# Kernel tuning notes

Measured on AMD Instinct MI355X. Metric: run time of the kernel, lower is better.

The kernel has to match this reference:

```python
import jax, jax.numpy as jnp
import numpy as np

N_NODES = 100000
N_EDGES = 1600000
IN_F = 256
OUT_F = 128


def setup_inputs() -> dict:
    key = jax.random.key(0)
    k1, k2, k3, k4, k5, k6 = jax.random.split(key, 6)
    x = jax.random.normal(k1, (N_NODES, IN_F), dtype=jnp.float32)
    edge_row = jax.random.randint(k2, (N_EDGES,), 0, N_NODES, dtype=jnp.int32)
    edge_col = jax.random.randint(k3, (N_EDGES,), 0, N_NODES, dtype=jnp.int32)
    edge_val = jax.random.uniform(k4, (N_EDGES,), dtype=jnp.float32)
    # xavier_uniform for W: bound = sqrt(6/(fan_in+fan_out))
    bound_w = float(np.sqrt(6.0 / (IN_F + OUT_F)))
    W = jax.random.uniform(k5, (IN_F, OUT_F), dtype=jnp.float32, minval=-bound_w, maxval=bound_w)
    stdv = 1.0 / float(np.sqrt(OUT_F))
    b = jax.random.uniform(k6, (OUT_F,), dtype=jnp.float32, minval=-stdv, maxval=stdv)
    return {"x": x, "edge_row": edge_row, "edge_col": edge_col, "edge_val": edge_val, "W": W, "b": b}


def reference(x, edge_row, edge_col, edge_val, W, b):
    # dropout p=0.0 -> identity
    support = x @ W + b                      # [N, out]
    # sparse adjacency matmul: out[r] += val * support[c] over edges (r, c, val)
    msgs = edge_val[:, None] * support[edge_col]          # [E, out]
    out = jax.ops.segment_sum(msgs, edge_row, num_segments=N_NODES)  # [N, out]
    return jax.nn.relu(out)
```

## Files before the change

### kernel.cpp

```cpp
#include <hip/hip_runtime.h>


constexpr int kNodes = 100000;
constexpr int kEdges = 1600000;
constexpr int kInF   = 256;
constexpr int kOutF  = 128;
constexpr int kTiles = kNodes / 16;
constexpr int kGemmBlocks = 1250;

constexpr int kNB  = 1024;
constexpr int kRB  = 98;
constexpr int kCap = 1792;
constexpr int kBinBlocks = 256;
constexpr int kEPB = kEdges / kBinBlocks;

constexpr int kTileCap = 1024;

typedef __attribute__((ext_vector_type(8))) short short8;
typedef __attribute__((ext_vector_type(8))) unsigned short ush8;
typedef __attribute__((ext_vector_type(4))) float floatx4;

__device__ inline unsigned short f2bf_rne(float f) {
    unsigned int u = __float_as_uint(f);
    unsigned int r = u + 0x7FFFu + ((u >> 16) & 1u);
    return (unsigned short)(r >> 16);
}
__device__ inline float bf2f(unsigned short h) {
    return __uint_as_float(((unsigned int)h) << 16);
}

__device__ inline short8 cvt8_bf16(const float4 a, const float4 b) {
    union { short8 s; unsigned int u[4]; } r;
    asm("v_cvt_pk_bf16_f32 %0, %1, %2" : "=v"(r.u[0]) : "v"(a.x), "v"(a.y));
    asm("v_cvt_pk_bf16_f32 %0, %1, %2" : "=v"(r.u[1]) : "v"(a.z), "v"(a.w));
    asm("v_cvt_pk_bf16_f32 %0, %1, %2" : "=v"(r.u[2]) : "v"(b.x), "v"(b.y));
    asm("v_cvt_pk_bf16_f32 %0, %1, %2" : "=v"(r.u[3]) : "v"(b.z), "v"(b.w));
    return r.s;
}

__device__ inline void gload_lds16(const void* g, void* l) {
    __builtin_amdgcn_global_load_lds(
        (const __attribute__((address_space(1))) unsigned int*)g,
        (__attribute__((address_space(3))) unsigned int*)l,
        16, 0, 0);
}

__global__ __launch_bounds__(256) void gcn_gemm(const float* __restrict__ x,
                                                const float* __restrict__ W,
                                                const float* __restrict__ b,
                                                unsigned short* __restrict__ support) {
    __shared__ __align__(16) float lbuf[2][4096];

    const int lane = threadIdx.x & 63;
    const int wv   = threadIdx.x >> 6;
    const int rowl = lane & 15;
    const int quad = lane >> 4;
    const int colbase = wv * 32;

    short8 bfrag[2][8];
#pragma unroll
    for (int ct = 0; ct < 2; ++ct) {
        const int col = colbase + ct * 16 + rowl;
#pragma unroll
        for (int kc = 0; kc < 8; ++kc) {
            const int kb = kc * 32 + quad * 8;
            short8 f;
#pragma unroll
            for (int j = 0; j < 8; ++j)
                f[j] = (short)f2bf_rne(W[(size_t)(kb + j) * kOutF + col]);
            bfrag[ct][kc] = f;
        }
    }
    const float bias0 = b[colbase + rowl];
    const float bias1 = b[colbase + 16 + rowl];

    const int G = gridDim.x;
    int t = blockIdx.x;

#define GEMM_STAGE(buf_, tile_)                                                   \
    do {                                                                          \
        const float* tb_ = x + (size_t)(tile_) * 16 * kInF;                       \
        _Pragma("unroll")                                                         \
        for (int i_ = 0; i_ < 4; ++i_) {                                          \
            const int row_ = i_ * 4 + wv;                                         \
            gload_lds16(tb_ + (size_t)row_ * kInF + ((lane ^ (row_ & 7)) << 2),   \
                        &lbuf[buf_][row_ << 8]);                                  \
        }                                                                         \
    } while (0)

    if (t < kTiles) GEMM_STAGE(0, t);
    int cur = 0;

    for (; t < kTiles; t += G) {
        const int tn = t + G;
        asm volatile("s_waitcnt vmcnt(0)" ::: "memory");
        __syncthreads();
        if (tn < kTiles) GEMM_STAGE(cur ^ 1, tn);

        const int r0 = t * 16;
        const float* base = &lbuf[cur][rowl << 8];
        const int rsw = rowl & 7;
        floatx4 acc0 = {0.f, 0.f, 0.f, 0.f};
        floatx4 acc1 = {0.f, 0.f, 0.f, 0.f};
#pragma unroll
        for (int kc = 0; kc < 8; ++kc) {
            const int g0 = (kc << 3) + (quad << 1);
            const float4 v0 = *reinterpret_cast<const float4*>(base + ((g0 ^ rsw) << 2));
            const float4 v1 = *reinterpret_cast<const float4*>(base + (((g0 + 1) ^ rsw) << 2));
            const short8 a = cvt8_bf16(v0, v1);
            acc0 = __builtin_amdgcn_mfma_f32_16x16x32_bf16(a, bfrag[0][kc], acc0, 0, 0, 0);
            acc1 = __builtin_amdgcn_mfma_f32_16x16x32_bf16(a, bfrag[1][kc], acc1, 0, 0, 0);
        }
#pragma unroll
        for (int reg = 0; reg < 4; ++reg) {
            const size_t rbase = (size_t)(r0 + quad * 4 + reg) * kOutF + colbase;
            support[rbase + rowl]      = f2bf_rne(acc0[reg] + bias0);
            support[rbase + 16 + rowl] = f2bf_rne(acc1[reg] + bias1);
        }
        cur ^= 1;
    }
#undef GEMM_STAGE
}

__global__ __launch_bounds__(256) void gcn_bhist(const int* __restrict__ erow,
                                                 int* __restrict__ bucket_tot) {
    __shared__ int cnt[kNB];
    const int tid = threadIdx.x;
    for (int i = tid; i < kNB; i += 256) cnt[i] = 0;
    __syncthreads();
    const int eb0 = blockIdx.x * kEPB;
    const int eb1 = min(eb0 + kEPB, kEdges);
    for (int e = eb0 + tid; e < eb1; e += 256)
        atomicAdd(&cnt[(unsigned int)erow[e] / (unsigned int)kRB], 1);
    __syncthreads();
    for (int i = tid; i < kNB; i += 256) {
        const int c = cnt[i];
        if (c) atomicAdd(&bucket_tot[i], c);
    }
}

__global__ __launch_bounds__(256) void gcn_bscan(const int* __restrict__ bucket_tot,
                                                 int* __restrict__ bucket_base,
                                                 int* __restrict__ cursor,
                                                 int* __restrict__ row_start) {
    __shared__ int s[kNB];
    const int tid = threadIdx.x;
    int t[4];
#pragma unroll
    for (int j = 0; j < 4; ++j) {
        const int idx = tid + j * 256;
        t[j] = bucket_tot[idx];
        s[idx] = t[j];
    }
    __syncthreads();
    for (int off = 1; off < kNB; off <<= 1) {
        int v[4];
#pragma unroll
        for (int j = 0; j < 4; ++j) {
            const int idx = tid + j * 256;
            v[j] = (idx >= off) ? s[idx - off] : 0;
        }
        __syncthreads();
#pragma unroll
        for (int j = 0; j < 4; ++j) s[tid + j * 256] += v[j];
        __syncthreads();
    }
#pragma unroll
    for (int j = 0; j < 4; ++j) {
        const int idx = tid + j * 256;
        const int excl = s[idx] - t[j];
        bucket_base[idx] = excl;
        cursor[idx]      = excl;
    }
    if (tid == 255) {
        bucket_base[kNB]  = kEdges;
        row_start[kNodes] = kEdges;
    }
}

__global__ __launch_bounds__(256) void gcn_bin(const int* __restrict__ erow,
                                               const int* __restrict__ ecol,
                                               const float* __restrict__ eval,
                                               int* __restrict__ cursor,
                                               int2* __restrict__ packed) {
    __shared__ int cnt[kNB];
    __shared__ int rk[kNB];
    const int tid = threadIdx.x;
    const int eb0 = blockIdx.x * kEPB;
    const int eb1 = min(eb0 + kEPB, kEdges);
    for (int i = tid; i < kNB; i += 256) { cnt[i] = 0; rk[i] = 0; }
    __syncthreads();
#pragma unroll 4
    for (int e = eb0 + tid; e < eb1; e += 256)
        atomicAdd(&cnt[(unsigned int)erow[e] / (unsigned int)kRB], 1);
    __syncthreads();
    for (int i = tid; i < kNB; i += 256) {
        const int c = cnt[i];
        cnt[i] = c ? atomicAdd(&cursor[i], c) : 0;
    }
    __syncthreads();
#pragma unroll 4
    for (int e = eb0 + tid; e < eb1; e += 256) {
        const int r = erow[e];
        const unsigned int bk = (unsigned int)r / (unsigned int)kRB;
        const int rl = r - (int)bk * kRB;
        const int pos = cnt[bk] + atomicAdd(&rk[bk], 1);
        packed[pos] = make_int2((rl << 17) | ecol[e], __float_as_int(eval[e]));
    }
}

__global__ __launch_bounds__(256) void gcn_place(const int* __restrict__ bucket_base,
                                                 int* __restrict__ row_start,
                                                 int2* __restrict__ packed) {
    __shared__ int2 st[kCap];
    __shared__ int  s[128];
    __shared__ int  rcur[kRB];
    const int bk = blockIdx.x;
    const int r0 = bk * kRB;
    if (r0 >= kNodes) return;
    const int r1 = min(r0 + kRB, kNodes);
    const int NR = r1 - r0;
    const int bb = bucket_base[bk];
    const int s1 = bucket_base[bk + 1];
    const int size   = s1 - bb;
    const int staged = min(size, kCap);
    const int tid = threadIdx.x;

    if (tid < 128) s[tid] = 0;
    __syncthreads();

    for (int i = tid; i < staged; i += 256) {
        const int2 p = packed[bb + i];
        st[i] = p;
        atomicAdd(&s[p.x >> 17], 1);
    }
    int2 tail[8];
    int  nt = 0;
    for (int i = kCap + tid; i < size; i += 256) {
        if (nt < 8) {
            tail[nt] = packed[bb + i];
            atomicAdd(&s[tail[nt].x >> 17], 1);
            ++nt;
        }
    }
    __syncthreads();

    for (int off = 1; off < 128; off <<= 1) {
        int v = 0;
        if (tid < 128 && tid >= off) v = s[tid - off];
        __syncthreads();
        if (tid < 128) s[tid] += v;
        __syncthreads();
    }
    if (tid < NR) {
        const int excl = tid ? s[tid - 1] : 0;
        row_start[r0 + tid] = bb + excl;
        rcur[tid] = excl;
    }
    __syncthreads();

    for (int i = tid; i < staged; i += 256) {
        const int2 p  = st[i];
        const int pos = bb + atomicAdd(&rcur[p.x >> 17], 1);
        packed[pos] = make_int2(p.x & 0x1FFFF, p.y);
    }
#pragma unroll
    for (int t = 0; t < 8; ++t) {
        if (t < nt) {
            const int2 p  = tail[t];
            const int pos = bb + atomicAdd(&rcur[p.x >> 17], 1);
            packed[pos] = make_int2(p.x & 0x1FFFF, p.y);
        }
    }
}

__global__ __launch_bounds__(256) void gcn_aggregate(const int* __restrict__ row_start,
                                                     const int2* __restrict__ packed,
                                                     const unsigned short* __restrict__ support,
                                                     float* __restrict__ out) {
    __shared__ int2 ep[kTileCap];
    const int n0 = blockIdx.x * 16;
    const int e0 = row_start[n0];
    const int eN = row_start[n0 + 16] - e0;
    const int nStage = min(eN, kTileCap);
    for (int i = threadIdx.x; i < nStage; i += 256)
        ep[i] = packed[e0 + i];
    __syncthreads();

    const int n  = n0 + (threadIdx.x >> 4);
    const int f8 = (threadIdx.x & 15) * 8;
    const unsigned short* sb = support + f8;
    const int s0 = row_start[n]     - e0;
    const int s1 = row_start[n + 1] - e0;

    float acc[8];
#pragma unroll
    for (int j = 0; j < 8; ++j) acc[j] = 0.f;

    if (eN <= kTileCap) {
        int i = s0;
        for (; i + 7 < s1; i += 8) {
            int2 p[8];
#pragma unroll
            for (int k = 0; k < 8; ++k) p[k] = ep[i + k];
            ush8 g[8];
#pragma unroll
            for (int k = 0; k < 8; ++k)
                g[k] = *reinterpret_cast<const ush8*>(sb + (size_t)p[k].x * kOutF);
#pragma unroll
            for (int k = 0; k < 8; ++k) {
                const float v = __int_as_float(p[k].y);
#pragma unroll
                for (int j = 0; j < 8; ++j) acc[j] += v * bf2f(g[k][j]);
            }
        }
        for (; i < s1; ++i) {
            const int2 p = ep[i];
            const float v = __int_as_float(p.y);
            const ush8 g = *reinterpret_cast<const ush8*>(sb + (size_t)p.x * kOutF);
#pragma unroll
            for (int j = 0; j < 8; ++j) acc[j] += v * bf2f(g[j]);
        }
    } else {
        int i = s0;
        for (; i + 3 < s1; i += 4) {
            const int2 p0 = packed[e0 + i];
            const int2 p1 = packed[e0 + i + 1];
            const int2 p2 = packed[e0 + i + 2];
            const int2 p3 = packed[e0 + i + 3];
            const ush8 a0 = *reinterpret_cast<const ush8*>(sb + (size_t)p0.x * kOutF);
            const ush8 a1 = *reinterpret_cast<const ush8*>(sb + (size_t)p1.x * kOutF);
            const ush8 a2 = *reinterpret_cast<const ush8*>(sb + (size_t)p2.x * kOutF);
            const ush8 a3 = *reinterpret_cast<const ush8*>(sb + (size_t)p3.x * kOutF);
            const float v0 = __int_as_float(p0.y), v1 = __int_as_float(p1.y);
            const float v2 = __int_as_float(p2.y), v3 = __int_as_float(p3.y);
#pragma unroll
            for (int j = 0; j < 8; ++j) {
                acc[j] += v0 * bf2f(a0[j]);
                acc[j] += v1 * bf2f(a1[j]);
                acc[j] += v2 * bf2f(a2[j]);
                acc[j] += v3 * bf2f(a3[j]);
            }
        }
        for (; i < s1; ++i) {
            const int2 p = packed[e0 + i];
            const float v = __int_as_float(p.y);
            const ush8 a = *reinterpret_cast<const ush8*>(sb + (size_t)p.x * kOutF);
#pragma unroll
            for (int j = 0; j < 8; ++j) acc[j] += v * bf2f(a[j]);
        }
    }

    float4 o0 = make_float4(fmaxf(acc[0], 0.f), fmaxf(acc[1], 0.f),
                            fmaxf(acc[2], 0.f), fmaxf(acc[3], 0.f));
    float4 o1 = make_float4(fmaxf(acc[4], 0.f), fmaxf(acc[5], 0.f),
                            fmaxf(acc[6], 0.f), fmaxf(acc[7], 0.f));
    *reinterpret_cast<float4*>(out + (size_t)n * kOutF + f8)     = o0;
    *reinterpret_cast<float4*>(out + (size_t)n * kOutF + f8 + 4) = o1;
}

extern "C" void kernel_launch(void* const* d_in, const int* in_sizes, int n_in,
                              void* d_out, int out_size, void* d_ws, size_t ws_size,
                              hipStream_t stream) {
    const float* x    = (const float*)d_in[0];
    const int*   erow = (const int*)  d_in[1];
    const int*   ecol = (const int*)  d_in[2];
    const float* eval = (const float*)d_in[3];
    const float* W    = (const float*)d_in[4];
    const float* b    = (const float*)d_in[5];
    float* out = (float*)d_out;

    char* ws = (char*)d_ws;
    unsigned short* support = (unsigned short*)(ws);
    int2* packed      = (int2*)(ws + 25600000);
    int*  row_start   = (int*) (ws + 38400000);
    int*  bucket_tot  = (int*) (ws + 38800008);
    int*  bucket_base = (int*) (ws + 38804104);
    int*  cursor      = (int*) (ws + 38808204);

    gcn_gemm<<<kGemmBlocks, 256, 0, stream>>>(x, W, b, support);

    hipMemsetAsync(bucket_tot, 0, kNB * sizeof(int), stream);
    gcn_bhist<<<kBinBlocks, 256, 0, stream>>>(erow, bucket_tot);
    gcn_bscan<<<1, 256, 0, stream>>>(bucket_tot, bucket_base, cursor, row_start);
    gcn_bin  <<<kBinBlocks, 256, 0, stream>>>(erow, ecol, eval, cursor, packed);
    gcn_place<<<kNB, 256, 0, stream>>>(bucket_base, row_start, packed);

    gcn_aggregate<<<kTiles, 256, 0, stream>>>(row_start, packed, support, out);
}
```

Baseline: 331.5 us.

## Split GEMM tiles across the binning kernels to overlap compute with sorting

Removes the standalone GEMM launch and spreads its row tiles over the four CSR-build kernels (histogram, scan, bin, place). Each of these kernels gets extra blocks that run a slice of the GEMM, so the dense compute fills the idle CUs left by the small, latency-bound sorting stages. Every fused kernel now uses 32KB of dynamic shared memory, which may lower occupancy for the binning blocks. The per-stage tile splits are hand-tuned constants.

```diff
diff --git a/kernel.cpp b/kernel.cpp
--- a/kernel.cpp
+++ b/kernel.cpp
@@ -6,7 +6,6 @@
 constexpr int kInF   = 256;
 constexpr int kOutF  = 128;
 constexpr int kTiles = kNodes / 16;
-constexpr int kGemmBlocks = 1250;
 
 constexpr int kNB  = 1024;
 constexpr int kRB  = 98;
@@ -15,6 +14,10 @@
 constexpr int kEPB = kEdges / kBinBlocks;
 
 constexpr int kTileCap = 1024;
+
+constexpr int kC1 = 1600, kC2 = 1900, kC3 = 4700, kC4 = kTiles;
+constexpr int kG1 = 320, kG2 = 64, kG3 = 560, kG4 = 312;
+constexpr int kSmem = 32768;
 
 typedef __attribute__((ext_vector_type(8))) short short8;
 typedef __attribute__((ext_vector_type(8))) unsigned short ush8;
@@ -45,12 +48,11 @@
         16, 0, 0);
 }
 
-__global__ __launch_bounds__(256) void gcn_gemm(const float* __restrict__ x,
-                                                const float* __restrict__ W,
-                                                const float* __restrict__ b,
-                                                unsigned short* __restrict__ support) {
-    __shared__ __align__(16) float lbuf[2][4096];
-
+__device__ inline void gemm_body(const float* __restrict__ x,
+                                 const float* __restrict__ W,
+                                 const float* __restrict__ b,
+                                 unsigned short* __restrict__ support,
+                                 float* lbuf, int t0, int t1, int gblk, int nG) {
     const int lane = threadIdx.x & 63;
     const int wv   = threadIdx.x >> 6;
     const int rowl = lane & 15;
@@ -74,31 +76,31 @@
     const float bias0 = b[colbase + rowl];
     const float bias1 = b[colbase + 16 + rowl];
 
-    const int G = gridDim.x;
-    int t = blockIdx.x;
-
-#define GEMM_STAGE(buf_, tile_)                                                   \
+    float* bcur = lbuf;
+    float* bnxt = lbuf + 4096;
+
+#define GEMM_STAGE(dst_, tile_)                                                   \
     do {                                                                          \
         const float* tb_ = x + (size_t)(tile_) * 16 * kInF;                       \
         _Pragma("unroll")                                                         \
         for (int i_ = 0; i_ < 4; ++i_) {                                          \
             const int row_ = i_ * 4 + wv;                                         \
             gload_lds16(tb_ + (size_t)row_ * kInF + ((lane ^ (row_ & 7)) << 2),   \
-                        &lbuf[buf_][row_ << 8]);                                  \
+                        (dst_) + (row_ << 8));                                    \
         }                                                                         \
     } while (0)
 
-    if (t < kTiles) GEMM_STAGE(0, t);
-    int cur = 0;
-
-    for (; t < kTiles; t += G) {
-        const int tn = t + G;
+    int t = t0 + gblk;
+    if (t < t1) GEMM_STAGE(bcur, t);
+
+    for (; t < t1; t += nG) {
+        const int tn = t + nG;
         asm volatile("s_waitcnt vmcnt(0)" ::: "memory");
         __syncthreads();
-        if (tn < kTiles) GEMM_STAGE(cur ^ 1, tn);
+        if (tn < t1) GEMM_STAGE(bnxt, tn);
 
         const int r0 = t * 16;
-        const float* base = &lbuf[cur][rowl << 8];
+        const float* base = bcur + (rowl << 8);
         const int rsw = rowl & 7;
         floatx4 acc0 = {0.f, 0.f, 0.f, 0.f};
         floatx4 acc1 = {0.f, 0.f, 0.f, 0.f};
@@ -117,14 +119,13 @@
             support[rbase + rowl]      = f2bf_rne(acc0[reg] + bias0);
             support[rbase + 16 + rowl] = f2bf_rne(acc1[reg] + bias1);
         }
-        cur ^= 1;
+        float* tmp = bcur; bcur = bnxt; bnxt = tmp;
     }
 #undef GEMM_STAGE
 }
 
-__global__ __launch_bounds__(256) void gcn_bhist(const int* __restrict__ erow,
-                                                 int* __restrict__ bucket_tot) {
-    __shared__ int cnt[kNB];
+__device__ inline void bhist_body(const int* __restrict__ erow,
+                                  int* __restrict__ bucket_tot, int* cnt) {
     const int tid = threadIdx.x;
     for (int i = tid; i < kNB; i += 256) cnt[i] = 0;
     __syncthreads();
@@ -139,11 +140,10 @@
     }
 }
 
-__global__ __launch_bounds__(256) void gcn_bscan(const int* __restrict__ bucket_tot,
-                                                 int* __restrict__ bucket_base,
-                                                 int* __restrict__ cursor,
-                                                 int* __restrict__ row_start) {
-    __shared__ int s[kNB];
+__device__ inline void bscan_body(const int* __restrict__ bucket_tot,
+                                  int* __restrict__ bucket_base,
+                                  int* __restrict__ cursor,
+                                  int* __restrict__ row_start, int* s) {
     const int tid = threadIdx.x;
     int t[4];
 #pragma unroll
@@ -178,13 +178,11 @@
     }
 }
 
-__global__ __launch_bounds__(256) void gcn_bin(const int* __restrict__ erow,
-                                               const int* __restrict__ ecol,
-                                               const float* __restrict__ eval,
-                                               int* __restrict__ cursor,
-                                               int2* __restrict__ packed) {
-    __shared__ int cnt[kNB];
-    __shared__ int rk[kNB];
+__device__ inline void bin_body(const int* __restrict__ erow,
+                                const int* __restrict__ ecol,
+                                const float* __restrict__ eval,
+                                int* __restrict__ cursor,
+                                int2* __restrict__ packed, int* cnt, int* rk) {
     const int tid = threadIdx.x;
     const int eb0 = blockIdx.x * kEPB;
     const int eb1 = min(eb0 + kEPB, kEdges);
@@ -209,12 +207,12 @@
     }
 }
 
-__global__ __launch_bounds__(256) void gcn_place(const int* __restrict__ bucket_base,
-                                                 int* __restrict__ row_start,
-                                                 int2* __restrict__ packed) {
-    __shared__ int2 st[kCap];
-    __shared__ int  s[128];
-    __shared__ int  rcur[kRB];
+__device__ inline void place_body(const int* __restrict__ bucket_base,
+                                  int* __restrict__ row_start,
+                                  int2* __restrict__ packed, char* smem) {
+    int2* st   = (int2*)smem;
+    int*  s    = (int*)(smem + 14336);
+    int*  rcur = (int*)(smem + 14848);
     const int bk = blockIdx.x;
     const int r0 = bk * kRB;
     if (r0 >= kNodes) return;
@@ -272,6 +270,64 @@
             packed[pos] = make_int2(p.x & 0x1FFFF, p.y);
         }
     }
+}
+
+__global__ __launch_bounds__(256) void gcn_k1(const float* __restrict__ x,
+                                              const float* __restrict__ W,
+                                              const float* __restrict__ b,
+                                              unsigned short* __restrict__ support,
+                                              const int* __restrict__ erow,
+                                              int* __restrict__ bucket_tot) {
+    extern __shared__ char smem[];
+    if (blockIdx.x < kBinBlocks)
+        bhist_body(erow, bucket_tot, (int*)smem);
+    else
+        gemm_body(x, W, b, support, (float*)smem, 0, kC1, blockIdx.x - kBinBlocks, kG1);
+}
+
+__global__ __launch_bounds__(256) void gcn_k2(const float* __restrict__ x,
+                                              const float* __restrict__ W,
+                                              const float* __restrict__ b,
+                                              unsigned short* __restrict__ support,
+                                              const int* __restrict__ bucket_tot,
+                                              int* __restrict__ bucket_base,
+                                              int* __restrict__ cursor,
+                                              int* __restrict__ row_start) {
+    extern __shared__ char smem[];
+    if (blockIdx.x == 0)
+        bscan_body(bucket_tot, bucket_base, cursor, row_start, (int*)smem);
+    else
+        gemm_body(x, W, b, support, (float*)smem, kC1, kC2, blockIdx.x - 1, kG2);
+}
+
+__global__ __launch_bounds__(256) void gcn_k3(const float* __restrict__ x,
+                                              const float* __restrict__ W,
+                                              const float* __restrict__ b,
+                                              unsigned short* __restrict__ support,
+                                              const int* __restrict__ erow,
+                                              const int* __restrict__ ecol,
+                                              const float* __restrict__ eval,
+                                              int* __restrict__ cursor,
+                                              int2* __restrict__ packed) {
+    extern __shared__ char smem[];
+    if (blockIdx.x < kBinBlocks)
+        bin_body(erow, ecol, eval, cursor, packed, (int*)smem, (int*)(smem + 4096));
+    else
+        gemm_body(x, W, b, support, (float*)smem, kC2, kC3, blockIdx.x - kBinBlocks, kG3);
+}
+
+__global__ __launch_bounds__(256) void gcn_k4(const float* __restrict__ x,
+                                              const float* __restrict__ W,
+                                              const float* __restrict__ b,
+                                              unsigned short* __restrict__ support,
+                                              const int* __restrict__ bucket_base,
+                                              int* __restrict__ row_start,
+                                              int2* __restrict__ packed) {
+    extern __shared__ char smem[];
+    if (blockIdx.x < kNB)
+        place_body(bucket_base, row_start, packed, smem);
+    else
+        gemm_body(x, W, b, support, (float*)smem, kC3, kC4, blockIdx.x - kNB, kG4);
 }
 
 __global__ __launch_bounds__(256) void gcn_aggregate(const int* __restrict__ row_start,
@@ -378,13 +434,15 @@
     int*  bucket_base = (int*) (ws + 38804104);
     int*  cursor      = (int*) (ws + 38808204);
 
-    gcn_gemm<<<kGemmBlocks, 256, 0, stream>>>(x, W, b, support);
-
     hipMemsetAsync(bucket_tot, 0, kNB * sizeof(int), stream);
-    gcn_bhist<<<kBinBlocks, 256, 0, stream>>>(erow, bucket_tot);
-    gcn_bscan<<<1, 256, 0, stream>>>(bucket_tot, bucket_base, cursor, row_start);
-    gcn_bin  <<<kBinBlocks, 256, 0, stream>>>(erow, ecol, eval, cursor, packed);
-    gcn_place<<<kNB, 256, 0, stream>>>(bucket_base, row_start, packed);
+
+    gcn_k1<<<kBinBlocks + kG1, 256, kSmem, stream>>>(x, W, b, support, erow, bucket_tot);
+    gcn_k2<<<1 + kG2,          256, kSmem, stream>>>(x, W, b, support, bucket_tot,
+                                                     bucket_base, cursor, row_start);
+    gcn_k3<<<kBinBlocks + kG3, 256, kSmem, stream>>>(x, W, b, support, erow, ecol, eval,
+                                                     cursor, packed);
+    gcn_k4<<<kNB + kG4,        256, kSmem, stream>>>(x, W, b, support, bucket_base,
+                                                     row_start, packed);
 
     gcn_aggregate<<<kTiles, 256, 0, stream>>>(row_start, packed, support, out);
 }
```

After: 365.5 us. 1.1x slower.

## Fuse histogram into GEMM and aggregate buckets via LDS atomics, dropping row sort

Applied to the files above, without the earlier changes.

The edge-bucket histogram moves into the GEMM kernel, so one launch and one pass over edge rows go away. The per-row placement kernel and the row-sorted aggregate are replaced by a single bucket-level kernel. It accumulates each 98-row bucket in an LDS tile with float atomicAdds, then applies ReLU and writes out. This removes the second reorder pass and the row_start array, but adds LDS atomic contention and a large LDS footprint (about 52KB) that limits occupancy. It also gives up the register-accumulated per-row gather.

```diff
diff --git a/kernel.cpp b/kernel.cpp
--- a/kernel.cpp
+++ b/kernel.cpp
@@ -7,14 +7,13 @@
 constexpr int kOutF  = 128;
 constexpr int kTiles = kNodes / 16;
 constexpr int kGemmBlocks = 1250;
+constexpr int kEPG = kEdges / kGemmBlocks;
 
 constexpr int kNB  = 1024;
 constexpr int kRB  = 98;
-constexpr int kCap = 1792;
+constexpr int kNBu = (kNodes + kRB - 1) / kRB;
 constexpr int kBinBlocks = 256;
 constexpr int kEPB = kEdges / kBinBlocks;
-
-constexpr int kTileCap = 1024;
 
 typedef __attribute__((ext_vector_type(8))) short short8;
 typedef __attribute__((ext_vector_type(8))) unsigned short ush8;
@@ -48,14 +47,32 @@
 __global__ __launch_bounds__(256) void gcn_gemm(const float* __restrict__ x,
                                                 const float* __restrict__ W,
                                                 const float* __restrict__ b,
-                                                unsigned short* __restrict__ support) {
+                                                unsigned short* __restrict__ support,
+                                                const int* __restrict__ erow,
+                                                int* __restrict__ bucket_tot) {
     __shared__ __align__(16) float lbuf[2][4096];
-
-    const int lane = threadIdx.x & 63;
-    const int wv   = threadIdx.x >> 6;
+    __shared__ int cnt[kNB];
+
+    const int tid  = threadIdx.x;
+    const int lane = tid & 63;
+    const int wv   = tid >> 6;
     const int rowl = lane & 15;
     const int quad = lane >> 4;
     const int colbase = wv * 32;
+
+    for (int i = tid; i < kNB; i += 256) cnt[i] = 0;
+    __syncthreads();
+    {
+        const int eb0 = blockIdx.x * kEPG;
+        const int eb1 = min(eb0 + kEPG, kEdges);
+        for (int e = eb0 + tid; e < eb1; e += 256)
+            atomicAdd(&cnt[(unsigned int)erow[e] / (unsigned int)kRB], 1);
+    }
+    __syncthreads();
+    for (int i = tid; i < kNB; i += 256) {
+        const int c = cnt[i];
+        if (c) atomicAdd(&bucket_tot[i], c);
+    }
 
     short8 bfrag[2][8];
 #pragma unroll
@@ -122,27 +139,9 @@
 #undef GEMM_STAGE
 }
 
-__global__ __launch_bounds__(256) void gcn_bhist(const int* __restrict__ erow,
-                                                 int* __restrict__ bucket_tot) {
-    __shared__ int cnt[kNB];
-    const int tid = threadIdx.x;
-    for (int i = tid; i < kNB; i += 256) cnt[i] = 0;
-    __syncthreads();
-    const int eb0 = blockIdx.x * kEPB;
-    const int eb1 = min(eb0 + kEPB, kEdges);
-    for (int e = eb0 + tid; e < eb1; e += 256)
-        atomicAdd(&cnt[(unsigned int)erow[e] / (unsigned int)kRB], 1);
-    __syncthreads();
-    for (int i = tid; i < kNB; i += 256) {
-        const int c = cnt[i];
-        if (c) atomicAdd(&bucket_tot[i], c);
-    }
-}
-
 __global__ __launch_bounds__(256) void gcn_bscan(const int* __restrict__ bucket_tot,
                                                  int* __restrict__ bucket_base,
-                                                 int* __restrict__ cursor,
-                                                 int* __restrict__ row_start) {
+                                                 int* __restrict__ cursor) {
     __shared__ int s[kNB];
     const int tid = threadIdx.x;
     int t[4];
@@ -172,10 +171,7 @@
         bucket_base[idx] = excl;
         cursor[idx]      = excl;
     }
-    if (tid == 255) {
-        bucket_base[kNB]  = kEdges;
-        row_start[kNodes] = kEdges;
-    }
+    if (tid == 255) bucket_base[kNB] = kEdges;
 }
 
 __global__ __launch_bounds__(256) void gcn_bin(const int* __restrict__ erow,
@@ -209,154 +205,57 @@
     }
 }
 
-__global__ __launch_bounds__(256) void gcn_place(const int* __restrict__ bucket_base,
-                                                 int* __restrict__ row_start,
-                                                 int2* __restrict__ packed) {
-    __shared__ int2 st[kCap];
-    __shared__ int  s[128];
-    __shared__ int  rcur[kRB];
+__global__ __launch_bounds__(256) void gcn_aggscat(const int* __restrict__ bucket_base,
+                                                   const int2* __restrict__ packed,
+                                                   const unsigned short* __restrict__ support,
+                                                   float* __restrict__ out) {
+    __shared__ float acc[kRB][132];
+    __shared__ int2  stg[256];
     const int bk = blockIdx.x;
     const int r0 = bk * kRB;
-    if (r0 >= kNodes) return;
-    const int r1 = min(r0 + kRB, kNodes);
-    const int NR = r1 - r0;
+    const int NR = min(kRB, kNodes - r0);
+    const int tid = threadIdx.x;
+    const int grp = tid >> 4;
+    const int gl  = tid & 15;
+
+    for (int i = tid; i < kRB * 132; i += 256)
+        (&acc[0][0])[i] = 0.f;
+
     const int bb = bucket_base[bk];
-    const int s1 = bucket_base[bk + 1];
-    const int size   = s1 - bb;
-    const int staged = min(size, kCap);
-    const int tid = threadIdx.x;
-
-    if (tid < 128) s[tid] = 0;
-    __syncthreads();
-
-    for (int i = tid; i < staged; i += 256) {
-        const int2 p = packed[bb + i];
-        st[i] = p;
-        atomicAdd(&s[p.x >> 17], 1);
-    }
-    int2 tail[8];
-    int  nt = 0;
-    for (int i = kCap + tid; i < size; i += 256) {
-        if (nt < 8) {
-            tail[nt] = packed[bb + i];
-            atomicAdd(&s[tail[nt].x >> 17], 1);
-            ++nt;
-        }
-    }
-    __syncthreads();
-
-    for (int off = 1; off < 128; off <<= 1) {
-        int v = 0;
-        if (tid < 128 && tid >= off) v = s[tid - off];
-        __syncthreads();
-        if (tid < 128) s[tid] += v;
-        __syncthreads();
-    }
-    if (tid < NR) {
-        const int excl = tid ? s[tid - 1] : 0;
-        row_start[r0 + tid] = bb + excl;
-        rcur[tid] = excl;
-    }
-    __syncthreads();
-
-    for (int i = tid; i < staged; i += 256) {
-        const int2 p  = st[i];
-        const int pos = bb + atomicAdd(&rcur[p.x >> 17], 1);
-        packed[pos] = make_int2(p.x & 0x1FFFF, p.y);
-    }
-#pragma unroll
-    for (int t = 0; t < 8; ++t) {
-        if (t < nt) {
-            const int2 p  = tail[t];
-            const int pos = bb + atomicAdd(&rcur[p.x >> 17], 1);
-            packed[pos] = make_int2(p.x & 0x1FFFF, p.y);
-        }
-    }
-}
-
-__global__ __launch_bounds__(256) void gcn_aggregate(const int* __restrict__ row_start,
-                                                     const int2* __restrict__ packed,
-                                                     const unsigned short* __restrict__ support,
-                                                     float* __restrict__ out) {
-    __shared__ int2 ep[kTileCap];
-    const int n0 = blockIdx.x * 16;
-    const int e0 = row_start[n0];
-    const int eN = row_start[n0 + 16] - e0;
-    const int nStage = min(eN, kTileCap);
-    for (int i = threadIdx.x; i < nStage; i += 256)
-        ep[i] = packed[e0 + i];
-    __syncthreads();
-
-    const int n  = n0 + (threadIdx.x >> 4);
-    const int f8 = (threadIdx.x & 15) * 8;
-    const unsigned short* sb = support + f8;
-    const int s0 = row_start[n]     - e0;
-    const int s1 = row_start[n + 1] - e0;
-
-    float acc[8];
-#pragma unroll
-    for (int j = 0; j < 8; ++j) acc[j] = 0.f;
-
-    if (eN <= kTileCap) {
-        int i = s0;
-        for (; i + 7 < s1; i += 8) {
-            int2 p[8];
-#pragma unroll
-            for (int k = 0; k < 8; ++k) p[k] = ep[i + k];
-            ush8 g[8];
-#pragma unroll
-            for (int k = 0; k < 8; ++k)
-                g[k] = *reinterpret_cast<const ush8*>(sb + (size_t)p[k].x * kOutF);
-#pragma unroll
-            for (int k = 0; k < 8; ++k) {
-                const float v = __int_as_float(p[k].y);
-#pragma unroll
-                for (int j = 0; j < 8; ++j) acc[j] += v * bf2f(g[k][j]);
+    const int be = bucket_base[bk + 1];
+    const unsigned short* sb = support + gl * 8;
+
+    for (int base = bb; base < be; base += 256) {
+        const int m = min(256, be - base);
+        __syncthreads();
+        if (tid < m) stg[tid] = packed[base + tid];
+        __syncthreads();
+#pragma unroll 4
+        for (int it = 0; it < 16; ++it) {
+            const int ei = it * 16 + grp;
+            if (ei < m) {
+                const int2 p = stg[ei];
+                const int rl = p.x >> 17;
+                const float v = __int_as_float(p.y);
+                const ush8 g = *reinterpret_cast<const ush8*>(
+                    sb + (size_t)(p.x & 0x1FFFF) * kOutF);
+                float* a = &acc[rl][gl * 8];
+#pragma unroll
+                for (int j = 0; j < 8; ++j)
+                    atomicAdd(&a[j], v * bf2f(g[j]));
             }
         }
-        for (; i < s1; ++i) {
-            const int2 p = ep[i];
-            const float v = __int_as_float(p.y);
-            const ush8 g = *reinterpret_cast<const ush8*>(sb + (size_t)p.x * kOutF);
-#pragma unroll
-            for (int j = 0; j < 8; ++j) acc[j] += v * bf2f(g[j]);
-        }
-    } else {
-        int i = s0;
-        for (; i + 3 < s1; i += 4) {
-            const int2 p0 = packed[e0 + i];
-            const int2 p1 = packed[e0 + i + 1];
-            const int2 p2 = packed[e0 + i + 2];
-            const int2 p3 = packed[e0 + i + 3];
-            const ush8 a0 = *reinterpret_cast<const ush8*>(sb + (size_t)p0.x * kOutF);
-            const ush8 a1 = *reinterpret_cast<const ush8*>(sb + (size_t)p1.x * kOutF);
-            const ush8 a2 = *reinterpret_cast<const ush8*>(sb + (size_t)p2.x * kOutF);
-            const ush8 a3 = *reinterpret_cast<const ush8*>(sb + (size_t)p3.x * kOutF);
-            const float v0 = __int_as_float(p0.y), v1 = __int_as_float(p1.y);
-            const float v2 = __int_as_float(p2.y), v3 = __int_as_float(p3.y);
-#pragma unroll
-            for (int j = 0; j < 8; ++j) {
-                acc[j] += v0 * bf2f(a0[j]);
-                acc[j] += v1 * bf2f(a1[j]);
-                acc[j] += v2 * bf2f(a2[j]);
-                acc[j] += v3 * bf2f(a3[j]);
-            }
-        }
-        for (; i < s1; ++i) {
-            const int2 p = packed[e0 + i];
-            const float v = __int_as_float(p.y);
-            const ush8 a = *reinterpret_cast<const ush8*>(sb + (size_t)p.x * kOutF);
-#pragma unroll
-            for (int j = 0; j < 8; ++j) acc[j] += v * bf2f(a[j]);
-        }
-    }
-
-    float4 o0 = make_float4(fmaxf(acc[0], 0.f), fmaxf(acc[1], 0.f),
-                            fmaxf(acc[2], 0.f), fmaxf(acc[3], 0.f));
-    float4 o1 = make_float4(fmaxf(acc[4], 0.f), fmaxf(acc[5], 0.f),
-                            fmaxf(acc[6], 0.f), fmaxf(acc[7], 0.f));
-    *reinterpret_cast<float4*>(out + (size_t)n * kOutF + f8)     = o0;
-    *reinterpret_cast<float4*>(out + (size_t)n * kOutF + f8 + 4) = o1;
+    }
+    __syncthreads();
+
+    for (int idx = tid; idx < NR * 32; idx += 256) {
+        const int r = idx >> 5;
+        const int c = (idx & 31) * 4;
+        const float4 a4 = *reinterpret_cast<const float4*>(&acc[r][c]);
+        const float4 o = make_float4(fmaxf(a4.x, 0.f), fmaxf(a4.y, 0.f),
+                                     fmaxf(a4.z, 0.f), fmaxf(a4.w, 0.f));
+        *reinterpret_cast<float4*>(out + (size_t)(r0 + r) * kOutF + c) = o;
+    }
 }
 
 extern "C" void kernel_launch(void* const* d_in, const int* in_sizes, int n_in,
@@ -373,18 +272,16 @@
     char* ws = (char*)d_ws;
     unsigned short* support = (unsigned short*)(ws);
     int2* packed      = (int2*)(ws + 25600000);
-    int*  row_start   = (int*) (ws + 38400000);
-    int*  bucket_tot  = (int*) (ws + 38800008);
-    int*  bucket_base = (int*) (ws + 38804104);
-    int*  cursor      = (int*) (ws + 38808204);
-
-    gcn_gemm<<<kGemmBlocks, 256, 0, stream>>>(x, W, b, support);
+    int*  bucket_tot  = (int*) (ws + 38400000);
+    int*  bucket_base = (int*) (ws + 38404096);
+    int*  cursor      = (int*) (ws + 38408200);
 
     hipMemsetAsync(bucket_tot, 0, kNB * sizeof(int), stream);
-    gcn_bhist<<<kBinBlocks, 256, 0, stream>>>(erow, bucket_tot);
-    gcn_bscan<<<1, 256, 0, stream>>>(bucket_tot, bucket_base, cursor, row_start);
+
+    gcn_gemm<<<kGemmBlocks, 256, 0, stream>>>(x, W, b, support, erow, bucket_tot);
+
+    gcn_bscan<<<1, 256, 0, stream>>>(bucket_tot, bucket_base, cursor);
     gcn_bin  <<<kBinBlocks, 256, 0, stream>>>(erow, ecol, eval, cursor, packed);
-    gcn_place<<<kNB, 256, 0, stream>>>(bucket_base, row_start, packed);
-
-    gcn_aggregate<<<kTiles, 256, 0, stream>>>(row_start, packed, support, out);
-}
+
+    gcn_aggscat<<<kNBu, 256, 0, stream>>>(bucket_base, packed, support, out);
+}
```

After: 1.307 ms. 294% more time.
